# Optimization experiments

Hardware: AMD Instinct MI355X
Metric: run time of the kernel (lower is better)

Reference implementation:

```python
import jax, jax.numpy as jnp
import numpy as np

B, S, H = 8, 8192, 1024
CAPACITY_FACTOR = 0.5


def setup_inputs() -> dict:
    key = jax.random.key(0)
    ks = jax.random.split(key, 5)
    sc = lambda fan: np.float32(1.0 / np.sqrt(fan))
    return {
        "x": jax.random.normal(ks[0], (B, S, H), dtype=jnp.float32),
        # router: Linear(H, H//4) -> ReLU -> Linear(H//4, 1)
        "W1": jax.random.normal(ks[1], (H, H // 4), dtype=jnp.float32) * sc(H),
        "b1": jnp.zeros((H // 4,), dtype=jnp.float32),
        "W2": jax.random.normal(ks[2], (H // 4, 1), dtype=jnp.float32) * sc(H // 4),
        "b2": jnp.zeros((1,), dtype=jnp.float32),
        # external layer_fn realized as a dense layer: gelu(x @ Wl)
        "Wl": jax.random.normal(ks[3], (H, H), dtype=jnp.float32) * sc(H),
    }


def reference(x, W1, b1, W2, b2, Wl):
    # router scores [B, S, 1]
    scores = jax.nn.relu(jnp.einsum("bsh,hd->bsd", x, W1) + b1)
    scores = jnp.einsum("bsd,do->bso", scores, W2) + b2
    routing_weights = jax.nn.sigmoid(scores)  # [B, S, 1]

    # eval path: process only top-capacity tokens per batch row
    capacity = int(S * CAPACITY_FACTOR)
    _, top_idx = jax.lax.top_k(scores[..., 0], capacity)  # [B, C]

    selected = jnp.take_along_axis(x, top_idx[..., None], axis=1)  # [B, C, H]
    processed = jax.nn.gelu(jnp.einsum("bch,hd->bcd", selected, Wl))  # layer_fn

    batch_idx = jnp.arange(x.shape[0])[:, None]  # [B, 1]
    output = x.at[batch_idx, top_idx].set(processed)  # scatter back into clone of x
    return output, routing_weights
```

## Files before the change

### kernel.cpp

```cpp
#include <hip/hip_runtime.h>
#include <stdint.h>

#define B_   8
#define S_   8192
#define H_   1024
#define HQ_  256
#define CAP_ 4096
#define UCAP_ (S_-CAP_)
#define M_   (B_*CAP_)
#define EPSB 0.012f
#define LCAP 8192

using f32x4 = __attribute__((ext_vector_type(4))) float;
using s16x8 = __attribute__((ext_vector_type(8))) short;

__device__ __forceinline__ unsigned short f2bf(float f) {
  unsigned u = __float_as_uint(f);
  u += 0x7FFF + ((u >> 16) & 1);
  return (unsigned short)(u >> 16);
}
__device__ __forceinline__ float bf2f(unsigned short h) {
  return __uint_as_float(((unsigned)h) << 16);
}

__device__ __forceinline__ float gelu_f(float v) {
  float s = v + 0.044715f * v * v * v;
  float e = __expf(-1.5957691216057308f * s);
  return v * __builtin_amdgcn_rcpf(1.0f + e);
}

__device__ __forceinline__ unsigned mono(float f) {
  unsigned u = __float_as_uint(f);
  return (u & 0x80000000u) ? ~u : (u | 0x80000000u);
}
__device__ __forceinline__ float unmono(unsigned k) {
  unsigned u = (k & 0x80000000u) ? (k & 0x7fffffffu) : ~k;
  return __uint_as_float(u);
}

__device__ __forceinline__ void gload_lds16(const void* g, void* l) {
  __builtin_amdgcn_global_load_lds(
      (const __attribute__((address_space(1))) void*)(uintptr_t)g,
      (__attribute__((address_space(3))) void*)(uintptr_t)l,
      16, 0, 0);
}

__global__ __launch_bounds__(256) void prep_w1_kernel(
    const float* __restrict__ W1, unsigned short* __restrict__ w1t_hi) {
  __shared__ float tile[32][33];
  const int n0 = blockIdx.x * 32, k0 = blockIdx.y * 32;
  const int tx = threadIdx.x, ty = threadIdx.y;
  for (int i = ty; i < 32; i += 8) tile[i][tx] = W1[(size_t)(k0 + i) * HQ_ + n0 + tx];
  __syncthreads();
  for (int i = ty; i < 32; i += 8)
    w1t_hi[(size_t)(n0 + i) * H_ + k0 + tx] = f2bf(tile[tx][i]);
}

__global__ __launch_bounds__(512) void router_mfma_kernel(
    const float* __restrict__ x, const unsigned short* __restrict__ w1t_hi,
    const float* __restrict__ b1, const float* __restrict__ W2,
    const float* __restrict__ b2, float* __restrict__ scores,
    float* __restrict__ rw) {
  __shared__ __align__(16) unsigned short AsH[2][128 * 32];
  __shared__ __align__(16) unsigned short BsH[2][256 * 32];
  __shared__ float part[128][4];
  const int t = threadIdx.x;
  const int lane = t & 63, w = t >> 6;
  const int m0 = blockIdx.x * 128;
  const int wr = w >> 2, wc = w & 3;
  const int r16 = lane & 15, ks = lane >> 4;

  const float* aptr[2];
  int aso[2];
  #pragma unroll
  for (int u = 0; u < 2; ++u) {
    int idx = t + u * 512;
    int row = idx >> 3, q = idx & 7;
    aptr[u] = x + (size_t)(m0 + row) * H_ + q * 4;
    aso[u] = row * 32 + (((q >> 1) ^ (row & 3)) << 3) + (q & 1) * 4;
  }
  const unsigned short* bptr[2];
  int bdst[2];
  #pragma unroll
  for (int q = 0; q < 2; ++q) {
    int cc0 = (q * 8 + w) * 64;
    int g = cc0 + lane;
    int row = g >> 2, sl = g & 3;
    int slz = sl ^ (row & 3);
    bptr[q] = w1t_hi + (size_t)row * H_ + slz * 8;
    bdst[q] = cc0 * 8;
  }

  f32x4 acc[4][4];
  #pragma unroll
  for (int i = 0; i < 4; ++i)
    #pragma unroll
    for (int j = 0; j < 4; ++j) acc[i][j] = (f32x4){0.f, 0.f, 0.f, 0.f};

  {
    float4 av[2];
    #pragma unroll
    for (int u = 0; u < 2; ++u) av[u] = *(const float4*)(aptr[u]);
    #pragma unroll
    for (int q = 0; q < 2; ++q) gload_lds16(bptr[q], &BsH[0][bdst[q]]);
    #pragma unroll
    for (int u = 0; u < 2; ++u) {
      ushort4 hh;
      hh.x = f2bf(av[u].x); hh.y = f2bf(av[u].y);
      hh.z = f2bf(av[u].z); hh.w = f2bf(av[u].w);
      *(ushort4*)&AsH[0][aso[u]] = hh;
    }
    __syncthreads();
  }

  for (int kt = 0; kt < 32; ++kt) {
    const int cur = kt & 1;
    const int k1 = (kt + 1) * 32;
    const bool pf = (kt < 31);
    float4 av[2];
    if (pf) {
      #pragma unroll
      for (int u = 0; u < 2; ++u) av[u] = *(const float4*)(aptr[u] + k1);
      #pragma unroll
      for (int q = 0; q < 2; ++q) gload_lds16(bptr[q] + k1, &BsH[cur ^ 1][bdst[q]]);
    }
    s16x8 ah[4], bh[4];
    #pragma unroll
    for (int i = 0; i < 4; ++i) {
      int r = wr * 64 + i * 16 + r16;
      ah[i] = *(const s16x8*)&AsH[cur][r * 32 + (ks ^ (r & 3)) * 8];
    }
    #pragma unroll
    for (int j = 0; j < 4; ++j) {
      int r = wc * 64 + j * 16 + r16;
      bh[j] = *(const s16x8*)&BsH[cur][r * 32 + (ks ^ (r & 3)) * 8];
    }
    #pragma unroll
    for (int i = 0; i < 4; ++i)
      #pragma unroll
      for (int j = 0; j < 4; ++j)
        acc[i][j] = __builtin_amdgcn_mfma_f32_16x16x32_bf16(ah[i], bh[j], acc[i][j], 0, 0, 0);
    if (pf) {
      #pragma unroll
      for (int u = 0; u < 2; ++u) {
        ushort4 hh;
        hh.x = f2bf(av[u].x); hh.y = f2bf(av[u].y);
        hh.z = f2bf(av[u].z); hh.w = f2bf(av[u].w);
        *(ushort4*)&AsH[cur ^ 1][aso[u]] = hh;
      }
    }
    __syncthreads();
  }

  float b1v[4], w2v[4];
  #pragma unroll
  for (int j = 0; j < 4; ++j) {
    int n = wc * 64 + j * 16 + r16;
    b1v[j] = b1[n]; w2v[j] = W2[n];
  }
  const int g4 = lane >> 4;
  #pragma unroll
  for (int i = 0; i < 4; ++i) {
    #pragma unroll
    for (int r = 0; r < 4; ++r) {
      float p = 0.f;
      #pragma unroll
      for (int j = 0; j < 4; ++j) {
        float h = acc[i][j][r] + b1v[j];
        h = fmaxf(h, 0.f);
        p = fmaf(h, w2v[j], p);
      }
      p += __shfl_xor(p, 1);
      p += __shfl_xor(p, 2);
      p += __shfl_xor(p, 4);
      p += __shfl_xor(p, 8);
      if (r16 == 0) part[wr * 64 + i * 16 + g4 * 4 + r][wc] = p;
    }
  }
  __syncthreads();
  if (t < 128) {
    float sc = part[t][0] + part[t][1] + part[t][2] + part[t][3] + b2[0];
    scores[m0 + t] = sc;
    rw[m0 + t] = 1.f / (1.f + expf(-sc));
  }
}

__global__ __launch_bounds__(1024) void select_kernel(
    const float* __restrict__ scores, float* __restrict__ thr) {
  __shared__ unsigned hist[2048];
  __shared__ unsigned sh_b, sh_gt;
  const int b = blockIdx.x;
  const int tid = threadIdx.x;
  const float* srow = scores + (size_t)b * S_;
  unsigned prefix = 0; int plen = 0; unsigned rank = CAP_;
  #pragma unroll
  for (int round = 0; round < 3; ++round) {
    const int nb = (round < 2) ? 11 : 10;
    hist[tid] = 0; hist[tid + 1024] = 0;
    __syncthreads();
    for (int i = tid; i < S_; i += 1024) {
      unsigned k = mono(srow[i]);
      if (plen == 0 || (k >> (32 - plen)) == prefix) {
        unsigned bucket = (k << plen) >> (32 - nb);
        atomicAdd(&hist[bucket], 1u);
      }
    }
    __syncthreads();
    for (int s = 1; s < 2048; s <<= 1) {
      unsigned t0 = (tid + s < 2048) ? hist[tid + s] : 0;
      unsigned t1 = (tid + 1024 + s < 2048) ? hist[tid + 1024 + s] : 0;
      __syncthreads();
      hist[tid] += t0; hist[tid + 1024] += t1;
      __syncthreads();
    }
    #pragma unroll
    for (int h = 0; h < 2; ++h) {
      int i = tid + h * 1024;
      unsigned ge = hist[i];
      unsigned gt = (i < 2047) ? hist[i + 1] : 0;
      if (gt < rank && rank <= ge) { sh_b = (unsigned)i; sh_gt = gt; }
    }
    __syncthreads();
    prefix = (prefix << nb) | sh_b;
    plen += nb;
    rank -= sh_gt;
    __syncthreads();
  }
  if (tid == 0) thr[b] = unmono(prefix);
}

__global__ __launch_bounds__(256) void band_kernel(
    const float* __restrict__ scores, const float* __restrict__ thr,
    int* __restrict__ list, int* __restrict__ count) {
  int i = blockIdx.x * 256 + threadIdx.x;
  float s = scores[i];
  int b = i >> 13;
  if (fabsf(s - thr[b]) <= EPSB) {
    int p = atomicAdd(count, 1);
    if (p < LCAP) list[p] = i;
  }
}

__global__ __launch_bounds__(256) void recompute_kernel(
    const float* __restrict__ x, const float* __restrict__ W1,
    const float* __restrict__ b1, const float* __restrict__ W2,
    const float* __restrict__ b2, const int* __restrict__ list,
    const int* __restrict__ count, float* __restrict__ scores,
    float* __restrict__ rw) {
  __shared__ float xr[4][H_];
  __shared__ float red[4][4];
  int n = *count; if (n > LCAP) n = LCAP;
  const int j = threadIdx.x;
  for (int base = blockIdx.x * 4; base < n; base += gridDim.x * 4) {
    int nt = n - base; if (nt > 4) nt = 4;
    for (int tt = 0; tt < 4; ++tt) {
      int tok = list[base + ((tt < nt) ? tt : 0)];
      const float* xrow = x + (size_t)tok * H_;
      for (int k = j; k < H_; k += 256) xr[tt][k] = xrow[k];
    }
    __syncthreads();
    float a0 = 0.f, a1 = 0.f, a2 = 0.f, a3 = 0.f;
    for (int k = 0; k < H_; ++k) {
      float wv = W1[(size_t)k * HQ_ + j];
      a0 = fmaf(xr[0][k], wv, a0);
      a1 = fmaf(xr[1][k], wv, a1);
      a2 = fmaf(xr[2][k], wv, a2);
      a3 = fmaf(xr[3][k], wv, a3);
    }
    float aa[4] = {a0, a1, a2, a3};
    #pragma unroll
    for (int tt = 0; tt < 4; ++tt) {
      float h = fmaxf(aa[tt] + b1[j], 0.f);
      float v = h * W2[j];
      v += __shfl_xor(v, 1);  v += __shfl_xor(v, 2);  v += __shfl_xor(v, 4);
      v += __shfl_xor(v, 8);  v += __shfl_xor(v, 16); v += __shfl_xor(v, 32);
      if ((j & 63) == 0) red[tt][j >> 6] = v;
    }
    __syncthreads();
    if (j < nt) {
      int tok = list[base + j];
      float sc = red[j][0] + red[j][1] + red[j][2] + red[j][3] + b2[0];
      scores[tok] = sc;
      rw[tok] = 1.f / (1.f + expf(-sc));
    }
    __syncthreads();
  }
}

__global__ __launch_bounds__(1024) void compact_kernel(
    const float* __restrict__ scores, const float* __restrict__ thr,
    int* __restrict__ comp, int* __restrict__ ucomp) {
  __shared__ int wc_eq[16], wc_sel[16], red[16];
  const int b = blockIdx.x;
  const float T = thr[b];
  const float* srow = scores + (size_t)b * S_;
  const int tid = threadIdx.x, lane = tid & 63, wid = tid >> 6;

  int cgt = 0;
  #pragma unroll
  for (int c = 0; c < 8; ++c) cgt += (srow[c * 1024 + tid] > T) ? 1 : 0;
  cgt += __shfl_xor(cgt, 1);  cgt += __shfl_xor(cgt, 2);  cgt += __shfl_xor(cgt, 4);
  cgt += __shfl_xor(cgt, 8);  cgt += __shfl_xor(cgt, 16); cgt += __shfl_xor(cgt, 32);
  if (lane == 0) red[wid] = cgt;
  __syncthreads();
  int cnt_gt = 0;
  #pragma unroll
  for (int i = 0; i < 16; ++i) cnt_gt += red[i];
  const int need = CAP_ - cnt_gt;

  int* crow = comp + b * CAP_;
  int* urow = ucomp + b * UCAP_;
  int sel_base = 0, unsel_base = 0, eq_base = 0;
  __syncthreads();
  for (int c = 0; c < 8; ++c) {
    int idx = c * 1024 + tid;
    float s = srow[idx];
    bool gt = s > T, eq = (s == T);
    unsigned long long meq = __ballot(eq);
    if (lane == 0) wc_eq[wid] = __popcll(meq);
    __syncthreads();
    int eq_off = eq_base, eq_tot = 0;
    #pragma unroll
    for (int w2 = 0; w2 < 16; ++w2) { if (w2 < wid) eq_off += wc_eq[w2]; eq_tot += wc_eq[w2]; }
    int eqpos = eq_off + __popcll(meq & ((1ull << lane) - 1));
    bool take = gt || (eq && eqpos < need);
    unsigned long long mt = __ballot(take);
    if (lane == 0) wc_sel[wid] = __popcll(mt);
    __syncthreads();
    int sel_off = sel_base, sel_tot = 0;
    #pragma unroll
    for (int w2 = 0; w2 < 16; ++w2) { if (w2 < wid) sel_off += wc_sel[w2]; sel_tot += wc_sel[w2]; }
    if (take) {
      crow[sel_off + __popcll(mt & ((1ull << lane) - 1))] = idx;
    } else {
      int un_off = unsel_base + wid * 64 - (sel_off - sel_base);
      urow[un_off + __popcll(~mt & ((1ull << lane) - 1))] = idx;
    }
    sel_base += sel_tot; unsel_base += 1024 - sel_tot; eq_base += eq_tot;
    __syncthreads();
  }
}

__global__ __launch_bounds__(256) void copy_unsel_kernel(
    const float* __restrict__ x, const int* __restrict__ ucomp,
    float* __restrict__ out) {
  int i = blockIdx.x;
  int b = i >> 12, r = i & (UCAP_ - 1);
  int token = ucomp[b * UCAP_ + r];
  size_t row = (size_t)b * S_ + token;
  const float4* src = (const float4*)(x + row * H_);
  float4* dst = (float4*)(out + row * H_);
  dst[threadIdx.x] = src[threadIdx.x];
}

__global__ __launch_bounds__(256) void wlt_kernel(
    const float* __restrict__ wl, unsigned short* __restrict__ wlt) {
  __shared__ float tile[32][33];
  const int x0 = blockIdx.x * 32, y0 = blockIdx.y * 32;
  const int tx = threadIdx.x, ty = threadIdx.y;
  for (int i = ty; i < 32; i += 8) tile[i][tx] = wl[(size_t)(y0 + i) * H_ + x0 + tx];
  __syncthreads();
  for (int i = ty; i < 32; i += 8)
    wlt[(size_t)(x0 + i) * H_ + y0 + tx] = f2bf(tile[tx][i]);
}

__global__ __launch_bounds__(256) void gather_cast_kernel(
    const float* __restrict__ x, const int* __restrict__ comp,
    unsigned short* __restrict__ xg) {
  int tid = blockIdx.x * 256 + threadIdx.x;
  int rowc = tid >> 8;
  int c4 = tid & 255;
  int b = rowc >> 12, cc = rowc & (CAP_ - 1);
  int token = comp[b * CAP_ + cc];
  float4 v = *(const float4*)&x[((size_t)(b * S_ + token)) * H_ + c4 * 4];
  ushort4 o;
  o.x = f2bf(v.x); o.y = f2bf(v.y); o.z = f2bf(v.z); o.w = f2bf(v.w);
  *(ushort4*)&xg[(size_t)rowc * H_ + c4 * 4] = o;
}

__global__ __launch_bounds__(256) void moe_gemm_kernel(
    const unsigned short* __restrict__ xg, const unsigned short* __restrict__ wlt,
    const int* __restrict__ comp, float* __restrict__ out) {
  __shared__ __align__(16) unsigned short As[2][128 * 32];
  __shared__ __align__(16) unsigned short Bs[2][128 * 32];
  __shared__ int toks[128];
  const int t = threadIdx.x;
  const int lane = t & 63, w = t >> 6;
  const int bid = blockIdx.x;
  const int xcd = bid & 7, wl_ = bid >> 3;
  const int m0 = (xcd * 32 + (wl_ >> 3)) * 128;
  const int n0 = (wl_ & 7) * 128;
  const int bb = m0 >> 12;
  if (t < 128) toks[t] = comp[bb * CAP_ + (m0 & (CAP_ - 1)) + t];
  const int wr = w >> 1, wc = w & 1;
  const int r16 = lane & 15, ks = lane >> 4;

  const unsigned short *aP[2], *bP[2];
  int dst[2];
  #pragma unroll
  for (int u = 0; u < 2; ++u) {
    int c = u * 256 + t;
    int row = c >> 2, sl = c & 3;
    int slz = sl ^ (row & 3);
    aP[u] = xg + (size_t)(m0 + row) * H_ + slz * 8;
    bP[u] = wlt + (size_t)(n0 + row) * H_ + slz * 8;
    dst[u] = (u * 256 + w * 64) * 8;
  }

  f32x4 acc[4][4];
  #pragma unroll
  for (int i = 0; i < 4; ++i)
    #pragma unroll
    for (int j = 0; j < 4; ++j) acc[i][j] = (f32x4){0.f, 0.f, 0.f, 0.f};

  #pragma unroll
  for (int u = 0; u < 2; ++u) {
    gload_lds16(aP[u], &As[0][dst[u]]);
    gload_lds16(bP[u], &Bs[0][dst[u]]);
  }
  __syncthreads();

  for (int kt = 0; kt < 32; ++kt) {
    const int cur = kt & 1;
    const int k1 = (kt + 1) * 32;
    if (kt < 31) {
      #pragma unroll
      for (int u = 0; u < 2; ++u) {
        gload_lds16(aP[u] + k1, &As[cur ^ 1][dst[u]]);
        gload_lds16(bP[u] + k1, &Bs[cur ^ 1][dst[u]]);
      }
    }
    s16x8 af[4], bfr[4];
    #pragma unroll
    for (int i = 0; i < 4; ++i) {
      int r = wr * 64 + i * 16 + r16;
      af[i] = *(const s16x8*)&As[cur][r * 32 + (ks ^ (r & 3)) * 8];
    }
    #pragma unroll
    for (int j = 0; j < 4; ++j) {
      int r = wc * 64 + j * 16 + r16;
      bfr[j] = *(const s16x8*)&Bs[cur][r * 32 + (ks ^ (r & 3)) * 8];
    }
    #pragma unroll
    for (int i = 0; i < 4; ++i)
      #pragma unroll
      for (int j = 0; j < 4; ++j)
        acc[i][j] = __builtin_amdgcn_mfma_f32_16x16x32_bf16(af[i], bfr[j], acc[i][j], 0, 0, 0);
    __syncthreads();
  }

  #pragma unroll
  for (int i = 0; i < 4; ++i) {
    #pragma unroll
    for (int r = 0; r < 4; ++r) {
      int rl = wr * 64 + i * 16 + (lane >> 4) * 4 + r;
      int token = toks[rl];
      float* orow = out + ((size_t)(bb * S_ + token)) * H_ + n0 + wc * 64;
      #pragma unroll
      for (int j = 0; j < 4; ++j)
        orow[j * 16 + r16] = gelu_f(acc[i][j][r]);
    }
  }
}

extern "C" void kernel_launch(void* const* d_in, const int* in_sizes, int n_in,
                              void* d_out, int out_size, void* d_ws, size_t ws_size,
                              hipStream_t stream) {
  const float* x  = (const float*)d_in[0];
  const float* W1 = (const float*)d_in[1];
  const float* b1 = (const float*)d_in[2];
  const float* W2 = (const float*)d_in[3];
  const float* b2 = (const float*)d_in[4];
  const float* Wl = (const float*)d_in[5];
  float* out = (float*)d_out;
  float* rw  = out + (size_t)B_ * S_ * H_;

  char* ws = (char*)d_ws;
  float* scores        = (float*)ws;
  int*   comp          = (int*)(ws + (256 << 10));
  float* thr           = (float*)(ws + (384 << 10));
  int*   count         = (int*)(ws + (384 << 10) + 256);
  int*   list          = (int*)(ws + (384 << 10) + 512);
  int*   ucomp         = (int*)(ws + (448 << 10));
  unsigned short* wlt  = (unsigned short*)(ws + (1 << 20));
  unsigned short* xg   = (unsigned short*)(ws + (3 << 20));
  unsigned short* w1t_hi = xg;

  hipMemsetAsync(count, 0, sizeof(int), stream);
  hipLaunchKernelGGL(prep_w1_kernel, dim3(HQ_/32, H_/32), dim3(32, 8), 0, stream,
                     W1, w1t_hi);
  hipLaunchKernelGGL(router_mfma_kernel, dim3((B_*S_)/128), dim3(512), 0, stream,
                     x, w1t_hi, b1, W2, b2, scores, rw);
  hipLaunchKernelGGL(select_kernel, dim3(B_), dim3(1024), 0, stream, scores, thr);
  hipLaunchKernelGGL(band_kernel, dim3((B_*S_)/256), dim3(256), 0, stream,
                     scores, thr, list, count);
  hipLaunchKernelGGL(recompute_kernel, dim3(128), dim3(256), 0, stream,
                     x, W1, b1, W2, b2, list, count, scores, rw);
  hipLaunchKernelGGL(select_kernel, dim3(B_), dim3(1024), 0, stream, scores, thr);
  hipLaunchKernelGGL(compact_kernel, dim3(B_), dim3(1024), 0, stream,
                     scores, thr, comp, ucomp);
  hipLaunchKernelGGL(copy_unsel_kernel, dim3(B_*UCAP_), dim3(256), 0, stream,
                     x, ucomp, out);
  hipLaunchKernelGGL(wlt_kernel, dim3(H_/32, H_/32), dim3(32, 8), 0, stream, Wl, wlt);
  hipLaunchKernelGGL(gather_cast_kernel, dim3(M_*H_/4/256), dim3(256), 0, stream,
                     x, comp, xg);
  hipLaunchKernelGGL(moe_gemm_kernel, dim3((M_/128)*(H_/128)), dim3(256), 0, stream,
                     xg, wlt, comp, out);
}
```

Baseline: 427.7 us.

## Emit bf16 copy of x in router and gather rows inside MoE GEMM

```diff
diff --git a/kernel.cpp b/kernel.cpp
--- a/kernel.cpp
+++ b/kernel.cpp
@@ -60,7 +60,7 @@
     const float* __restrict__ x, const unsigned short* __restrict__ w1t_hi,
     const float* __restrict__ b1, const float* __restrict__ W2,
     const float* __restrict__ b2, float* __restrict__ scores,
-    float* __restrict__ rw) {
+    float* __restrict__ rw, unsigned short* __restrict__ xbf) {
   __shared__ __align__(16) unsigned short AsH[2][128 * 32];
   __shared__ __align__(16) unsigned short BsH[2][256 * 32];
   __shared__ float part[128][4];
@@ -71,12 +71,14 @@
   const int r16 = lane & 15, ks = lane >> 4;
 
   const float* aptr[2];
+  unsigned short* xbptr[2];
   int aso[2];
   #pragma unroll
   for (int u = 0; u < 2; ++u) {
     int idx = t + u * 512;
     int row = idx >> 3, q = idx & 7;
-    aptr[u] = x + (size_t)(m0 + row) * H_ + q * 4;
+    aptr[u]  = x + (size_t)(m0 + row) * H_ + q * 4;
+    xbptr[u] = xbf + (size_t)(m0 + row) * H_ + q * 4;
     aso[u] = row * 32 + (((q >> 1) ^ (row & 3)) << 3) + (q & 1) * 4;
   }
   const unsigned short* bptr[2];
@@ -109,6 +111,7 @@
       hh.x = f2bf(av[u].x); hh.y = f2bf(av[u].y);
       hh.z = f2bf(av[u].z); hh.w = f2bf(av[u].w);
       *(ushort4*)&AsH[0][aso[u]] = hh;
+      *(ushort4*)(xbptr[u]) = hh;
     }
     __syncthreads();
   }
@@ -147,6 +150,7 @@
         hh.x = f2bf(av[u].x); hh.y = f2bf(av[u].y);
         hh.z = f2bf(av[u].z); hh.w = f2bf(av[u].w);
         *(ushort4*)&AsH[cur ^ 1][aso[u]] = hh;
+        *(ushort4*)(xbptr[u] + k1) = hh;
       }
     }
     __syncthreads();
@@ -364,47 +368,39 @@
     wlt[(size_t)(x0 + i) * H_ + y0 + tx] = f2bf(tile[tx][i]);
 }
 
-__global__ __launch_bounds__(256) void gather_cast_kernel(
-    const float* __restrict__ x, const int* __restrict__ comp,
-    unsigned short* __restrict__ xg) {
-  int tid = blockIdx.x * 256 + threadIdx.x;
-  int rowc = tid >> 8;
-  int c4 = tid & 255;
-  int b = rowc >> 12, cc = rowc & (CAP_ - 1);
-  int token = comp[b * CAP_ + cc];
-  float4 v = *(const float4*)&x[((size_t)(b * S_ + token)) * H_ + c4 * 4];
-  ushort4 o;
-  o.x = f2bf(v.x); o.y = f2bf(v.y); o.z = f2bf(v.z); o.w = f2bf(v.w);
-  *(ushort4*)&xg[(size_t)rowc * H_ + c4 * 4] = o;
-}
-
-__global__ __launch_bounds__(256) void moe_gemm_kernel(
-    const unsigned short* __restrict__ xg, const unsigned short* __restrict__ wlt,
+__global__ __launch_bounds__(512) void moe_gemm_kernel(
+    const unsigned short* __restrict__ xbf, const unsigned short* __restrict__ wlt,
     const int* __restrict__ comp, float* __restrict__ out) {
-  __shared__ __align__(16) unsigned short As[2][128 * 32];
+  __shared__ __align__(16) unsigned short As[2][256 * 32];
   __shared__ __align__(16) unsigned short Bs[2][128 * 32];
-  __shared__ int toks[128];
+  __shared__ int toks[256];
   const int t = threadIdx.x;
   const int lane = t & 63, w = t >> 6;
   const int bid = blockIdx.x;
   const int xcd = bid & 7, wl_ = bid >> 3;
-  const int m0 = (xcd * 32 + (wl_ >> 3)) * 128;
+  const int m0 = (xcd * 16 + (wl_ >> 3)) * 256;
   const int n0 = (wl_ & 7) * 128;
   const int bb = m0 >> 12;
-  if (t < 128) toks[t] = comp[bb * CAP_ + (m0 & (CAP_ - 1)) + t];
+  if (t < 256) toks[t] = comp[bb * CAP_ + (m0 & (CAP_ - 1)) + t];
+  __syncthreads();
   const int wr = w >> 1, wc = w & 1;
   const int r16 = lane & 15, ks = lane >> 4;
 
-  const unsigned short *aP[2], *bP[2];
-  int dst[2];
+  const unsigned short *aP[2], *bP;
+  int adst[2], bdst;
   #pragma unroll
   for (int u = 0; u < 2; ++u) {
-    int c = u * 256 + t;
+    int c = u * 512 + t;
     int row = c >> 2, sl = c & 3;
     int slz = sl ^ (row & 3);
-    aP[u] = xg + (size_t)(m0 + row) * H_ + slz * 8;
-    bP[u] = wlt + (size_t)(n0 + row) * H_ + slz * 8;
-    dst[u] = (u * 256 + w * 64) * 8;
+    aP[u] = xbf + ((size_t)(bb * S_ + toks[row])) * H_ + slz * 8;
+    adst[u] = (u * 512 + w * 64) * 8;
+  }
+  {
+    int row = t >> 2, sl = t & 3;
+    int slz = sl ^ (row & 3);
+    bP = wlt + (size_t)(n0 + row) * H_ + slz * 8;
+    bdst = (w * 64) * 8;
   }
 
   f32x4 acc[4][4];
@@ -414,10 +410,8 @@
     for (int j = 0; j < 4; ++j) acc[i][j] = (f32x4){0.f, 0.f, 0.f, 0.f};
 
   #pragma unroll
-  for (int u = 0; u < 2; ++u) {
-    gload_lds16(aP[u], &As[0][dst[u]]);
-    gload_lds16(bP[u], &Bs[0][dst[u]]);
-  }
+  for (int u = 0; u < 2; ++u) gload_lds16(aP[u], &As[0][adst[u]]);
+  gload_lds16(bP, &Bs[0][bdst]);
   __syncthreads();
 
   for (int kt = 0; kt < 32; ++kt) {
@@ -425,10 +419,8 @@
     const int k1 = (kt + 1) * 32;
     if (kt < 31) {
       #pragma unroll
-      for (int u = 0; u < 2; ++u) {
-        gload_lds16(aP[u] + k1, &As[cur ^ 1][dst[u]]);
-        gload_lds16(bP[u] + k1, &Bs[cur ^ 1][dst[u]]);
-      }
+      for (int u = 0; u < 2; ++u) gload_lds16(aP[u] + k1, &As[cur ^ 1][adst[u]]);
+      gload_lds16(bP + k1, &Bs[cur ^ 1][bdst]);
     }
     s16x8 af[4], bfr[4];
     #pragma unroll
@@ -483,14 +475,14 @@
   int*   list          = (int*)(ws + (384 << 10) + 512);
   int*   ucomp         = (int*)(ws + (448 << 10));
   unsigned short* wlt  = (unsigned short*)(ws + (1 << 20));
-  unsigned short* xg   = (unsigned short*)(ws + (3 << 20));
-  unsigned short* w1t_hi = xg;
+  unsigned short* xbf  = (unsigned short*)(ws + (3 << 20));
+  unsigned short* w1t_hi = (unsigned short*)(ws + (3 << 20) + (132u << 20));
 
   hipMemsetAsync(count, 0, sizeof(int), stream);
   hipLaunchKernelGGL(prep_w1_kernel, dim3(HQ_/32, H_/32), dim3(32, 8), 0, stream,
                      W1, w1t_hi);
   hipLaunchKernelGGL(router_mfma_kernel, dim3((B_*S_)/128), dim3(512), 0, stream,
-                     x, w1t_hi, b1, W2, b2, scores, rw);
+                     x, w1t_hi, b1, W2, b2, scores, rw, xbf);
   hipLaunchKernelGGL(select_kernel, dim3(B_), dim3(1024), 0, stream, scores, thr);
   hipLaunchKernelGGL(band_kernel, dim3((B_*S_)/256), dim3(256), 0, stream,
                      scores, thr, list, count);
@@ -502,8 +494,6 @@
   hipLaunchKernelGGL(copy_unsel_kernel, dim3(B_*UCAP_), dim3(256), 0, stream,
                      x, ucomp, out);
   hipLaunchKernelGGL(wlt_kernel, dim3(H_/32, H_/32), dim3(32, 8), 0, stream, Wl, wlt);
-  hipLaunchKernelGGL(gather_cast_kernel, dim3(M_*H_/4/256), dim3(256), 0, stream,
-                     x, comp, xg);
-  hipLaunchKernelGGL(moe_gemm_kernel, dim3((M_/128)*(H_/128)), dim3(256), 0, stream,
-                     xg, wlt, comp, out);
-}
+  hipLaunchKernelGGL(moe_gemm_kernel, dim3((M_/256)*(H_/128)), dim3(512), 0, stream,
+                     xbf, wlt, comp, out);
+}
```

Result: slower. 443.5 us (+3.7%).

## Use a two-level LDS swizzle and hand-tuned waitcnt/barrier pipelining in router and GEMM

Applied to the files above, without the earlier changes.

```diff
diff --git a/kernel.cpp b/kernel.cpp
--- a/kernel.cpp
+++ b/kernel.cpp
@@ -43,6 +43,10 @@
       (const __attribute__((address_space(1))) void*)(uintptr_t)g,
       (__attribute__((address_space(3))) void*)(uintptr_t)l,
       16, 0, 0);
+}
+
+__device__ __forceinline__ int swz4(int row) {
+  return (row & 3) ^ ((row >> 2) & 3);
 }
 
 __global__ __launch_bounds__(256) void prep_w1_kernel(
@@ -77,18 +81,17 @@
     int idx = t + u * 512;
     int row = idx >> 3, q = idx & 7;
     aptr[u] = x + (size_t)(m0 + row) * H_ + q * 4;
-    aso[u] = row * 32 + (((q >> 1) ^ (row & 3)) << 3) + (q & 1) * 4;
+    aso[u] = row * 32 + (((q >> 1) ^ swz4(row)) << 3) + (q & 1) * 4;
   }
   const unsigned short* bptr[2];
   int bdst[2];
   #pragma unroll
-  for (int q = 0; q < 2; ++q) {
-    int cc0 = (q * 8 + w) * 64;
-    int g = cc0 + lane;
-    int row = g >> 2, sl = g & 3;
-    int slz = sl ^ (row & 3);
-    bptr[q] = w1t_hi + (size_t)row * H_ + slz * 8;
-    bdst[q] = cc0 * 8;
+  for (int u = 0; u < 2; ++u) {
+    int c = u * 512 + t;
+    int row = c >> 2, sl = c & 3;
+    int slz = sl ^ swz4(row);
+    bptr[u] = w1t_hi + (size_t)row * H_ + slz * 8;
+    bdst[u] = (u * 512 + w * 64) * 8;
   }
 
   f32x4 acc[4][4];
@@ -98,11 +101,11 @@
     for (int j = 0; j < 4; ++j) acc[i][j] = (f32x4){0.f, 0.f, 0.f, 0.f};
 
   {
+    #pragma unroll
+    for (int u = 0; u < 2; ++u) gload_lds16(bptr[u], &BsH[0][bdst[u]]);
     float4 av[2];
     #pragma unroll
     for (int u = 0; u < 2; ++u) av[u] = *(const float4*)(aptr[u]);
-    #pragma unroll
-    for (int q = 0; q < 2; ++q) gload_lds16(bptr[q], &BsH[0][bdst[q]]);
     #pragma unroll
     for (int u = 0; u < 2; ++u) {
       ushort4 hh;
@@ -114,26 +117,26 @@
   }
 
   for (int kt = 0; kt < 32; ++kt) {
-    const int cur = kt & 1;
+    const int cur = kt & 1, nxt = cur ^ 1;
     const int k1 = (kt + 1) * 32;
     const bool pf = (kt < 31);
     float4 av[2];
     if (pf) {
       #pragma unroll
+      for (int u = 0; u < 2; ++u) gload_lds16(bptr[u] + k1, &BsH[nxt][bdst[u]]);
+      #pragma unroll
       for (int u = 0; u < 2; ++u) av[u] = *(const float4*)(aptr[u] + k1);
-      #pragma unroll
-      for (int q = 0; q < 2; ++q) gload_lds16(bptr[q] + k1, &BsH[cur ^ 1][bdst[q]]);
     }
     s16x8 ah[4], bh[4];
     #pragma unroll
     for (int i = 0; i < 4; ++i) {
       int r = wr * 64 + i * 16 + r16;
-      ah[i] = *(const s16x8*)&AsH[cur][r * 32 + (ks ^ (r & 3)) * 8];
+      ah[i] = *(const s16x8*)&AsH[cur][r * 32 + (ks ^ swz4(r)) * 8];
     }
     #pragma unroll
     for (int j = 0; j < 4; ++j) {
       int r = wc * 64 + j * 16 + r16;
-      bh[j] = *(const s16x8*)&BsH[cur][r * 32 + (ks ^ (r & 3)) * 8];
+      bh[j] = *(const s16x8*)&BsH[cur][r * 32 + (ks ^ swz4(r)) * 8];
     }
     #pragma unroll
     for (int i = 0; i < 4; ++i)
@@ -141,15 +144,18 @@
       for (int j = 0; j < 4; ++j)
         acc[i][j] = __builtin_amdgcn_mfma_f32_16x16x32_bf16(ah[i], bh[j], acc[i][j], 0, 0, 0);
     if (pf) {
+      __builtin_amdgcn_sched_barrier(0);
       #pragma unroll
       for (int u = 0; u < 2; ++u) {
         ushort4 hh;
         hh.x = f2bf(av[u].x); hh.y = f2bf(av[u].y);
         hh.z = f2bf(av[u].z); hh.w = f2bf(av[u].w);
-        *(ushort4*)&AsH[cur ^ 1][aso[u]] = hh;
+        *(ushort4*)&AsH[nxt][aso[u]] = hh;
       }
     }
-    __syncthreads();
+    asm volatile("s_waitcnt lgkmcnt(0)" ::: "memory");
+    __builtin_amdgcn_s_barrier();
+    __builtin_amdgcn_sched_barrier(0);
   }
 
   float b1v[4], w2v[4];
@@ -401,7 +407,7 @@
   for (int u = 0; u < 2; ++u) {
     int c = u * 256 + t;
     int row = c >> 2, sl = c & 3;
-    int slz = sl ^ (row & 3);
+    int slz = sl ^ swz4(row);
     aP[u] = xg + (size_t)(m0 + row) * H_ + slz * 8;
     bP[u] = wlt + (size_t)(n0 + row) * H_ + slz * 8;
     dst[u] = (u * 256 + w * 64) * 8;
@@ -418,7 +424,9 @@
     gload_lds16(aP[u], &As[0][dst[u]]);
     gload_lds16(bP[u], &Bs[0][dst[u]]);
   }
-  __syncthreads();
+  asm volatile("s_waitcnt vmcnt(0)" ::: "memory");
+  __builtin_amdgcn_s_barrier();
+  __builtin_amdgcn_sched_barrier(0);
 
   for (int kt = 0; kt < 32; ++kt) {
     const int cur = kt & 1;
@@ -429,24 +437,30 @@
         gload_lds16(aP[u] + k1, &As[cur ^ 1][dst[u]]);
         gload_lds16(bP[u] + k1, &Bs[cur ^ 1][dst[u]]);
       }
-    }
+      asm volatile("s_waitcnt vmcnt(4)" ::: "memory");
+    } else {
+      asm volatile("s_waitcnt vmcnt(0)" ::: "memory");
+    }
+    __builtin_amdgcn_s_barrier();
+    __builtin_amdgcn_sched_barrier(0);
     s16x8 af[4], bfr[4];
     #pragma unroll
     for (int i = 0; i < 4; ++i) {
       int r = wr * 64 + i * 16 + r16;
-      af[i] = *(const s16x8*)&As[cur][r * 32 + (ks ^ (r & 3)) * 8];
+      af[i] = *(const s16x8*)&As[cur][r * 32 + (ks ^ swz4(r)) * 8];
     }
     #pragma unroll
     for (int j = 0; j < 4; ++j) {
       int r = wc * 64 + j * 16 + r16;
-      bfr[j] = *(const s16x8*)&Bs[cur][r * 32 + (ks ^ (r & 3)) * 8];
+      bfr[j] = *(const s16x8*)&Bs[cur][r * 32 + (ks ^ swz4(r)) * 8];
     }
     #pragma unroll
     for (int i = 0; i < 4; ++i)
       #pragma unroll
       for (int j = 0; j < 4; ++j)
         acc[i][j] = __builtin_amdgcn_mfma_f32_16x16x32_bf16(af[i], bfr[j], acc[i][j], 0, 0, 0);
-    __syncthreads();
+    __builtin_amdgcn_s_barrier();
+    __builtin_amdgcn_sched_barrier(0);
   }
 
   #pragma unroll
```

After: 427.3 us. About the same (-0.1%).
